# Kernel optimization log

Hardware: AMD Instinct MI355X
Metric: run time of the kernel (lower is better)

The kernel has to match this reference:

```python
import jax, jax.numpy as jnp
import numpy as np

TEMP = 0.07  # softmax temperature T


def _l2norm(x, axis=1, eps=1e-12):
    return x / jnp.clip(jnp.linalg.norm(x, axis=axis, keepdims=True), eps, None)


def setup_inputs() -> dict:
    key = jax.random.key(0)
    k1, k2, k3, k4 = jax.random.split(key, 4)
    B, K, D = 256, 8192, 128
    q = jax.random.normal(k1, (B, D), dtype=jnp.float32)
    ba_queue = _l2norm(jax.random.normal(k2, (K, D), dtype=jnp.float32))
    nonba_queue = _l2norm(jax.random.normal(k3, (K, D), dtype=jnp.float32))
    targets = jax.random.randint(k4, (B,), 0, 2, dtype=jnp.int64)
    return {"q": q, "ba_queue": ba_queue, "nonba_queue": nonba_queue, "targets": targets}


def reference(q, ba_queue, nonba_queue, targets):
    K = ba_queue.shape[0]
    # encoder output is L2-normalized; queues are detached buffers
    qn = _l2norm(q, axis=1)
    all_feature = jnp.concatenate([qn, ba_queue, nonba_queue], axis=0)  # [N, D]
    all_label = jnp.concatenate([
        targets.astype(jnp.int32),
        jnp.ones((K,), dtype=jnp.int32),
        jnp.zeros((K,), dtype=jnp.int32),
    ])  # [N]
    N = all_feature.shape[0]

    # [N, N] similarity logits
    sim = jnp.matmul(all_feature, all_feature.T) / TEMP
    logits = sim - jax.lax.stop_gradient(jnp.max(sim, axis=1, keepdims=True))

    # positive mask (same label), excluding self
    mask = (all_label[:, None] == all_label[None, :]).astype(jnp.float32)
    logits_mask = 1.0 - jnp.eye(N, dtype=jnp.float32)
    mask = mask * logits_mask

    exp_logits = jnp.exp(logits) * logits_mask
    log_prob = logits - jnp.log(jnp.sum(exp_logits, axis=1, keepdims=True))
    mean_log_prob_pos = jnp.sum(mask * log_prob, axis=1) / jnp.sum(mask, axis=1)
    return -jnp.mean(mean_log_prob_pos)
```

## Files before the change

kernel.cpp:

```cpp
#include <hip/hip_runtime.h>
#include <hip/hip_bf16.h>
#include <stdint.h>

#define TEMPERATURE 0.07f
#define SC 20.6099312f

constexpr int NQ = 256;
constexpr int KQ = 8192;
constexpr int D  = 128;
constexpr int N  = NQ + 2 * KQ;
constexpr int CS = 26;
constexpr int CS2 = CS * 2;
constexpr int BN = 128;
constexpr int RBM = N / 128;
constexpr int RBF = N / 256;

typedef float f32x16 __attribute__((ext_vector_type(16)));
typedef int   i32x4  __attribute__((ext_vector_type(4)));
typedef int   i32x8  __attribute__((ext_vector_type(8)));

constexpr size_t OFF_F32  = 0;
constexpr size_t OFF_8    = OFF_F32  + (size_t)NQ * D * 4;
constexpr size_t OFF_8S   = OFF_8    + (size_t)N * D;
constexpr size_t OFF_PART = OFF_8S   + (size_t)N * D;
constexpr size_t OFF_LP   = OFF_PART + (size_t)CS2 * N * 4;
constexpr size_t OFF_BSUM = OFF_LP   + (size_t)260 * 2 * 128 * 4;

#define MFMA8(a, b, c) __builtin_amdgcn_mfma_scale_f32_32x32x64_f8f6f4( \
    (a), (b), (c), 0, 0, 0, 0x7f7f7f7f, 0, 0x7f7f7f7f)

__global__ __launch_bounds__(256) void k_prep(const float* __restrict__ q,
                                              const float* __restrict__ ba,
                                              const float* __restrict__ nb,
                                              const long long* __restrict__ tgt,
                                              float* __restrict__ ff,
                                              unsigned char* __restrict__ fb8,
                                              unsigned char* __restrict__ fb8s,
                                              float* __restrict__ lp) {
    __shared__ float red[4][2][128];
    int wid = threadIdx.x >> 6, lane = threadIdx.x & 63;
    int rbase = blockIdx.x * 64 + wid * 16;
    float s0x = 0.f, s0y = 0.f, s1x = 0.f, s1y = 0.f;
    for (int i = 0; i < 16; ++i) {
        int r = rbase + i;
        const float* src = (r < NQ) ? (q + (size_t)r * D)
                         : (r < NQ + KQ) ? (ba + (size_t)(r - NQ) * D)
                         : (nb + (size_t)(r - NQ - KQ) * D);
        float2 v = *(const float2*)(src + lane * 2);
        float a = v.x, b = v.y;
        int lab;
        if (r < NQ) {
            float ss = a * a + b * b;
            #pragma unroll
            for (int m = 1; m < 64; m <<= 1) ss += __shfl_xor(ss, m);
            float scale = 1.0f / fmaxf(sqrtf(ss), 1e-12f);
            a *= scale; b *= scale;
            lab = (int)tgt[r];
            *(float2*)(ff + (size_t)r * D + lane * 2) = make_float2(a, b);
        } else {
            lab = (r < NQ + KQ) ? 1 : 0;
        }
        int w8  = __builtin_amdgcn_cvt_pk_fp8_f32(a, b, 0, false);
        int w8s = __builtin_amdgcn_cvt_pk_fp8_f32(a * SC, b * SC, 0, false);
        *(unsigned short*)(fb8  + (size_t)r * D + lane * 2) = (unsigned short)w8;
        *(unsigned short*)(fb8s + (size_t)r * D + lane * 2) = (unsigned short)w8s;
        if (lab) { s1x += a; s1y += b; } else { s0x += a; s0y += b; }
    }
    red[wid][0][lane * 2]     = s0x;
    red[wid][0][lane * 2 + 1] = s0y;
    red[wid][1][lane * 2]     = s1x;
    red[wid][1][lane * 2 + 1] = s1y;
    __syncthreads();
    int lab2 = threadIdx.x >> 7, d = threadIdx.x & 127;
    float s = red[0][lab2][d] + red[1][lab2][d] + red[2][lab2][d] + red[3][lab2][d];
    lp[((size_t)blockIdx.x * 2 + lab2) * 128 + d] = s;
}

__global__ __launch_bounds__(256, 4) void k_main(const unsigned char* __restrict__ fb8,
                                                 const unsigned char* __restrict__ fb8s,
                                                 float* __restrict__ part) {
    __shared__ __align__(16) unsigned char lds[2][BN * 128];
    const int bid = blockIdx.x;
    const int rb = bid / CS, cs = bid % CS;
    const int tid = threadIdx.x;
    const int lane = tid & 63;
    const int wid  = tid >> 6;
    const int wr = wid >> 1, wc = wid & 1;
    const int l31 = lane & 31, lhi = lane >> 5;
    const int rw = rb * 128 + wr * 64;

    int soff[4];
    #pragma unroll
    for (int i = 0; i < 4; ++i) {
        int flat = i * 256 + tid;
        int line = flat >> 4, p = flat & 15;
        int pl = p ^ (line & 15);
        soff[i] = (2 * line + (pl >> 3)) * 128 + (pl & 7) * 16;
    }

#define STAGE(T, B) { \
    const unsigned char* base_ = fb8 + ((size_t)(cs + (T) * CS)) * (BN * 128); \
    _Pragma("unroll") \
    for (int i_ = 0; i_ < 4; ++i_) \
        __builtin_amdgcn_global_load_lds( \
            (const __attribute__((address_space(1))) unsigned int*)(base_ + soff[i_]), \
            (__attribute__((address_space(3))) unsigned int*)(&lds[B][(i_ * 256 + tid) * 16]), \
            16, 0, 0); }

#define SYNC() { asm volatile("s_waitcnt vmcnt(0)" ::: "memory"); __builtin_amdgcn_s_barrier(); }

    i32x8 rf[2][2];
    #pragma unroll
    for (int rs = 0; rs < 2; ++rs)
        #pragma unroll
        for (int s = 0; s < 2; ++s)
            rf[rs][s] = *(const i32x8*)(fb8s + (size_t)(rw + rs * 32 + l31) * D + s * 64 + lhi * 32);

    f32x16 z16;
    #pragma unroll
    for (int e = 0; e < 16; ++e) z16[e] = 0.f;

    float2 ps2[2] = {{0.f, 0.f}, {0.f, 0.f}};

    STAGE(0, 0) SYNC()

    #pragma unroll 1
    for (int t = 0; t < 5; ++t) {
        if (t + 1 < 5) STAGE(t + 1, (t & 1) ^ 1)
        const unsigned char* buf = &lds[t & 1][0];

        f32x16 acc[2][2];
        __builtin_amdgcn_s_setprio(1);
        #pragma unroll
        for (int s = 0; s < 2; ++s) {
            #pragma unroll
            for (int cc = 0; cc < 2; ++cc) {
                int crow = wc * 64 + cc * 32 + l31;
                int line = crow >> 1;
                int pb = ((crow & 1) << 3) + s * 4 + lhi * 2;
                const unsigned char* lb = buf + line * 256;
                i32x4 lo = *(const i32x4*)(lb + ((pb    ) ^ (line & 15)) * 16);
                i32x4 hi = *(const i32x4*)(lb + ((pb + 1) ^ (line & 15)) * 16);
                i32x8 a = {lo[0], lo[1], lo[2], lo[3], hi[0], hi[1], hi[2], hi[3]};
                acc[cc][0] = MFMA8(a, rf[0][s], (s == 0) ? z16 : acc[cc][0]);
                acc[cc][1] = MFMA8(a, rf[1][s], (s == 0) ? z16 : acc[cc][1]);
            }
        }
        __builtin_amdgcn_s_setprio(0);

        #pragma unroll
        for (int cc = 0; cc < 2; ++cc)
            #pragma unroll
            for (int rs = 0; rs < 2; ++rs) {
                float2 p = {0.f, 0.f};
                #pragma unroll
                for (int g = 0; g < 8; ++g) {
                    p.x += __builtin_amdgcn_exp2f(acc[cc][rs][2 * g]);
                    p.y += __builtin_amdgcn_exp2f(acc[cc][rs][2 * g + 1]);
                }
                ps2[rs].x += p.x; ps2[rs].y += p.y;
            }

        SYNC()
    }

    float rsum[2] = {ps2[0].x + ps2[0].y, ps2[1].x + ps2[1].y};
    rsum[0] += __shfl_xor(rsum[0], 32);
    rsum[1] += __shfl_xor(rsum[1], 32);
    if (lane < 32) {
        float* dst = part + (size_t)(cs * 2 + wc) * N + rw + lane;
        dst[0]  = rsum[0];
        dst[32] = rsum[1];
    }
#undef STAGE
#undef SYNC
}

__global__ __launch_bounds__(256) void k_rowfin(const float* __restrict__ part,
                                                const float* __restrict__ ff,
                                                const float* __restrict__ ba,
                                                const float* __restrict__ nb,
                                                const float* __restrict__ lp,
                                                const long long* __restrict__ tgt,
                                                float* __restrict__ bsum) {
    __shared__ float sS[256];
    __shared__ float red[256];
    __shared__ int scnt[2];
    {
        int lab = threadIdx.x >> 7, d = threadIdx.x & 127;
        float s[4] = {0.f, 0.f, 0.f, 0.f};
        for (int b = 0; b < 260; b += 4) {
            #pragma unroll
            for (int j = 0; j < 4; ++j)
                s[j] += lp[((size_t)(b + j) * 2 + lab) * 128 + d];
        }
        sS[threadIdx.x] = (s[0] + s[1]) + (s[2] + s[3]);
        if (threadIdx.x < 64) {
            int c = 0;
            #pragma unroll
            for (int i = 0; i < 4; ++i) c += (int)tgt[threadIdx.x + 64 * i];
            #pragma unroll
            for (int m = 1; m < 64; m <<= 1) c += __shfl_xor(c, m);
            if (threadIdx.x == 0) { scnt[0] = (NQ - c) + KQ; scnt[1] = c + KQ; }
        }
    }
    __syncthreads();
    int r = blockIdx.x * 256 + threadIdx.x;
    float se = 0.f;
    #pragma unroll 4
    for (int c = 0; c < CS2; ++c) se += part[(size_t)c * N + r];
    int lab = (r < NQ) ? (int)tgt[r] : ((r < NQ + KQ) ? 1 : 0);
    const float* fsrc = (r < NQ) ? (ff + (size_t)r * D)
                      : (r < NQ + KQ) ? (ba + (size_t)(r - NQ) * D)
                      : (nb + (size_t)(r - NQ - KQ) * D);
    const float4* frow = (const float4*)fsrc;
    const float4* srow = (const float4*)(sS + lab * 128);
    float dS = 0.f, dd = 0.f;
    #pragma unroll
    for (int i = 0; i < 32; ++i) {
        float4 f = frow[i];
        float4 s = srow[i];
        dS += f.x * s.x + f.y * s.y + f.z * s.z + f.w * s.w;
        int wa  = __builtin_amdgcn_cvt_pk_fp8_f32(f.x, f.y, 0, false);
        int wb  = __builtin_amdgcn_cvt_pk_fp8_f32(f.z, f.w, 0, false);
        int wsa = __builtin_amdgcn_cvt_pk_fp8_f32(f.x * SC, f.y * SC, 0, false);
        int wsb = __builtin_amdgcn_cvt_pk_fp8_f32(f.z * SC, f.w * SC, 0, false);
        dd += __builtin_amdgcn_cvt_f32_fp8(wa, 0) * __builtin_amdgcn_cvt_f32_fp8(wsa, 0)
            + __builtin_amdgcn_cvt_f32_fp8(wa, 1) * __builtin_amdgcn_cvt_f32_fp8(wsa, 1)
            + __builtin_amdgcn_cvt_f32_fp8(wb, 0) * __builtin_amdgcn_cvt_f32_fp8(wsb, 0)
            + __builtin_amdgcn_cvt_f32_fp8(wb, 1) * __builtin_amdgcn_cvt_f32_fp8(wsb, 1);
    }
    se -= __builtin_amdgcn_exp2f(dd);
    float lse = logf(se);
    float P = (float)(scnt[lab] - 1);
    float mlpp = (dS - 1.0f) / (TEMPERATURE * P) - lse;
    red[threadIdx.x] = mlpp;
    __syncthreads();
    for (int s2 = 128; s2 > 0; s2 >>= 1) {
        if (threadIdx.x < s2) red[threadIdx.x] += red[threadIdx.x + s2];
        __syncthreads();
    }
    if (threadIdx.x == 0) bsum[blockIdx.x] = red[0];
}

__global__ __launch_bounds__(64) void k_final(const float* __restrict__ bsum,
                                              float* __restrict__ out) {
    float s = bsum[threadIdx.x];
    if (threadIdx.x == 0) s += bsum[64];
    #pragma unroll
    for (int m = 1; m < 64; m <<= 1) s += __shfl_xor(s, m);
    if (threadIdx.x == 0) out[0] = -s / (float)N;
}

extern "C" void kernel_launch(void* const* d_in, const int* in_sizes, int n_in,
                              void* d_out, int out_size, void* d_ws, size_t ws_size,
                              hipStream_t stream) {
    const float* q       = (const float*)d_in[0];
    const float* ba      = (const float*)d_in[1];
    const float* nb      = (const float*)d_in[2];
    const long long* tgt = (const long long*)d_in[3];
    char* ws = (char*)d_ws;
    float*         ff   = (float*)(ws + OFF_F32);
    unsigned char* fb8  = (unsigned char*)(ws + OFF_8);
    unsigned char* fb8s = (unsigned char*)(ws + OFF_8S);
    float*         part = (float*)(ws + OFF_PART);
    float*         lp   = (float*)(ws + OFF_LP);
    float*         bsum = (float*)(ws + OFF_BSUM);

    k_prep  <<<260,      256, 0, stream>>>(q, ba, nb, tgt, ff, fb8, fb8s, lp);
    k_main  <<<RBM * CS, 256, 0, stream>>>(fb8, fb8s, part);
    k_rowfin<<<RBF,      256, 0, stream>>>(part, ff, ba, nb, lp, tgt, bsum);
    k_final <<<1,         64, 0, stream>>>(bsum, (float*)d_out);
}
```

Measured before the change: 82.23 us.

## Make each wave an independent job with private LDS buffers, removing block barriers

The main similarity kernel now gives each wavefront its own 64-row by column-split job, with a private double-buffered 4KB LDS stage in place of a 128x128 tile shared by the block. Block-wide barriers are gone and each wave waits only on its own loads through vmcnt counts. The number of column splits doubles to 52 and the grid grows to 3380 blocks. This drops per-tile barrier stalls and lets waves run out of sync, but it gives up sharing a staged tile across the four waves, so global and L2 traffic per MFMA rises.

```diff
diff --git a/kernel.cpp b/kernel.cpp
--- a/kernel.cpp
+++ b/kernel.cpp
@@ -9,10 +9,8 @@
 constexpr int KQ = 8192;
 constexpr int D  = 128;
 constexpr int N  = NQ + 2 * KQ;
-constexpr int CS = 26;
-constexpr int CS2 = CS * 2;
-constexpr int BN = 128;
-constexpr int RBM = N / 128;
+constexpr int CSW = 52;
+constexpr int NTW = 520 / CSW;
 constexpr int RBF = N / 256;
 
 typedef float f32x16 __attribute__((ext_vector_type(16)));
@@ -23,7 +21,7 @@
 constexpr size_t OFF_8    = OFF_F32  + (size_t)NQ * D * 4;
 constexpr size_t OFF_8S   = OFF_8    + (size_t)N * D;
 constexpr size_t OFF_PART = OFF_8S   + (size_t)N * D;
-constexpr size_t OFF_LP   = OFF_PART + (size_t)CS2 * N * 4;
+constexpr size_t OFF_LP   = OFF_PART + (size_t)CSW * N * 4;
 constexpr size_t OFF_BSUM = OFF_LP   + (size_t)260 * 2 * 128 * 4;
 
 #define MFMA8(a, b, c) __builtin_amdgcn_mfma_scale_f32_32x32x64_f8f6f4( \
@@ -79,35 +77,40 @@
 __global__ __launch_bounds__(256, 4) void k_main(const unsigned char* __restrict__ fb8,
                                                  const unsigned char* __restrict__ fb8s,
                                                  float* __restrict__ part) {
-    __shared__ __align__(16) unsigned char lds[2][BN * 128];
-    const int bid = blockIdx.x;
-    const int rb = bid / CS, cs = bid % CS;
+    __shared__ __align__(16) unsigned char lds[4][2][4096];
     const int tid = threadIdx.x;
     const int lane = tid & 63;
     const int wid  = tid >> 6;
-    const int wr = wid >> 1, wc = wid & 1;
+    const int job  = blockIdx.x * 4 + wid;
+    const int rg = job / CSW, cs = job % CSW;
     const int l31 = lane & 31, lhi = lane >> 5;
-    const int rw = rb * 128 + wr * 64;
+    const int rw = rg * 64;
+
+    unsigned char* myl = &lds[wid][0][0];
 
     int soff[4];
     #pragma unroll
     for (int i = 0; i < 4; ++i) {
-        int flat = i * 256 + tid;
-        int line = flat >> 4, p = flat & 15;
-        int pl = p ^ (line & 15);
-        soff[i] = (2 * line + (pl >> 3)) * 128 + (pl & 7) * 16;
+        int f = i * 64 + lane;
+        int row = f >> 3, pslot = f & 7;
+        soff[i] = row * 128 + ((pslot ^ (row & 7)) << 4);
+    }
+    int lofs[2][2];
+    #pragma unroll
+    for (int s = 0; s < 2; ++s) {
+        int p = s * 4 + lhi * 2;
+        lofs[s][0] = (l31 * 8 + ((p)     ^ (l31 & 7))) * 16;
+        lofs[s][1] = (l31 * 8 + ((p + 1) ^ (l31 & 7))) * 16;
     }
 
 #define STAGE(T, B) { \
-    const unsigned char* base_ = fb8 + ((size_t)(cs + (T) * CS)) * (BN * 128); \
+    const unsigned char* base_ = fb8 + ((size_t)(cs + (T) * CSW)) * 4096; \
     _Pragma("unroll") \
     for (int i_ = 0; i_ < 4; ++i_) \
         __builtin_amdgcn_global_load_lds( \
             (const __attribute__((address_space(1))) unsigned int*)(base_ + soff[i_]), \
-            (__attribute__((address_space(3))) unsigned int*)(&lds[B][(i_ * 256 + tid) * 16]), \
+            (__attribute__((address_space(3))) unsigned int*)(myl + (B) * 4096 + (i_ * 64 + lane) * 16), \
             16, 0, 0); }
-
-#define SYNC() { asm volatile("s_waitcnt vmcnt(0)" ::: "memory"); __builtin_amdgcn_s_barrier(); }
 
     i32x8 rf[2][2];
     #pragma unroll
@@ -122,58 +125,51 @@
 
     float2 ps2[2] = {{0.f, 0.f}, {0.f, 0.f}};
 
-    STAGE(0, 0) SYNC()
+    STAGE(0, 0)
 
     #pragma unroll 1
-    for (int t = 0; t < 5; ++t) {
-        if (t + 1 < 5) STAGE(t + 1, (t & 1) ^ 1)
-        const unsigned char* buf = &lds[t & 1][0];
-
-        f32x16 acc[2][2];
+    for (int t = 0; t < NTW; ++t) {
+        if (t + 1 < NTW) {
+            STAGE(t + 1, (t & 1) ^ 1)
+            asm volatile("s_waitcnt vmcnt(4)" ::: "memory");
+        } else {
+            asm volatile("s_waitcnt vmcnt(0)" ::: "memory");
+        }
+        const unsigned char* buf = myl + (t & 1) * 4096;
+
+        f32x16 acc[2];
         __builtin_amdgcn_s_setprio(1);
         #pragma unroll
         for (int s = 0; s < 2; ++s) {
-            #pragma unroll
-            for (int cc = 0; cc < 2; ++cc) {
-                int crow = wc * 64 + cc * 32 + l31;
-                int line = crow >> 1;
-                int pb = ((crow & 1) << 3) + s * 4 + lhi * 2;
-                const unsigned char* lb = buf + line * 256;
-                i32x4 lo = *(const i32x4*)(lb + ((pb    ) ^ (line & 15)) * 16);
-                i32x4 hi = *(const i32x4*)(lb + ((pb + 1) ^ (line & 15)) * 16);
-                i32x8 a = {lo[0], lo[1], lo[2], lo[3], hi[0], hi[1], hi[2], hi[3]};
-                acc[cc][0] = MFMA8(a, rf[0][s], (s == 0) ? z16 : acc[cc][0]);
-                acc[cc][1] = MFMA8(a, rf[1][s], (s == 0) ? z16 : acc[cc][1]);
+            i32x4 lo = *(const i32x4*)(buf + lofs[s][0]);
+            i32x4 hi = *(const i32x4*)(buf + lofs[s][1]);
+            i32x8 a = {lo[0], lo[1], lo[2], lo[3], hi[0], hi[1], hi[2], hi[3]};
+            acc[0] = MFMA8(a, rf[0][s], (s == 0) ? z16 : acc[0]);
+            acc[1] = MFMA8(a, rf[1][s], (s == 0) ? z16 : acc[1]);
+        }
+        __builtin_amdgcn_s_setprio(0);
+
+        #pragma unroll
+        for (int rs = 0; rs < 2; ++rs) {
+            float2 p = {0.f, 0.f};
+            #pragma unroll
+            for (int g = 0; g < 8; ++g) {
+                p.x += __builtin_amdgcn_exp2f(acc[rs][2 * g]);
+                p.y += __builtin_amdgcn_exp2f(acc[rs][2 * g + 1]);
             }
-        }
-        __builtin_amdgcn_s_setprio(0);
-
-        #pragma unroll
-        for (int cc = 0; cc < 2; ++cc)
-            #pragma unroll
-            for (int rs = 0; rs < 2; ++rs) {
-                float2 p = {0.f, 0.f};
-                #pragma unroll
-                for (int g = 0; g < 8; ++g) {
-                    p.x += __builtin_amdgcn_exp2f(acc[cc][rs][2 * g]);
-                    p.y += __builtin_amdgcn_exp2f(acc[cc][rs][2 * g + 1]);
-                }
-                ps2[rs].x += p.x; ps2[rs].y += p.y;
-            }
-
-        SYNC()
-    }
-
-    float rsum[2] = {ps2[0].x + ps2[0].y, ps2[1].x + ps2[1].y};
-    rsum[0] += __shfl_xor(rsum[0], 32);
-    rsum[1] += __shfl_xor(rsum[1], 32);
+            ps2[rs].x += p.x; ps2[rs].y += p.y;
+        }
+    }
+
+    float rsum0 = ps2[0].x + ps2[0].y;
+    float rsum1 = ps2[1].x + ps2[1].y;
+    rsum0 += __shfl_xor(rsum0, 32);
+    rsum1 += __shfl_xor(rsum1, 32);
     if (lane < 32) {
-        float* dst = part + (size_t)(cs * 2 + wc) * N + rw + lane;
-        dst[0]  = rsum[0];
-        dst[32] = rsum[1];
+        part[(size_t)cs * N + rw + lane]      = rsum0;
+        part[(size_t)cs * N + rw + 32 + lane] = rsum1;
     }
 #undef STAGE
-#undef SYNC
 }
 
 __global__ __launch_bounds__(256) void k_rowfin(const float* __restrict__ part,
@@ -208,7 +204,7 @@
     int r = blockIdx.x * 256 + threadIdx.x;
     float se = 0.f;
     #pragma unroll 4
-    for (int c = 0; c < CS2; ++c) se += part[(size_t)c * N + r];
+    for (int c = 0; c < CSW; ++c) se += part[(size_t)c * N + r];
     int lab = (r < NQ) ? (int)tgt[r] : ((r < NQ + KQ) ? 1 : 0);
     const float* fsrc = (r < NQ) ? (ff + (size_t)r * D)
                       : (r < NQ + KQ) ? (ba + (size_t)(r - NQ) * D)
@@ -267,8 +263,8 @@
     float*         lp   = (float*)(ws + OFF_LP);
     float*         bsum = (float*)(ws + OFF_BSUM);
 
-    k_prep  <<<260,      256, 0, stream>>>(q, ba, nb, tgt, ff, fb8, fb8s, lp);
-    k_main  <<<RBM * CS, 256, 0, stream>>>(fb8, fb8s, part);
-    k_rowfin<<<RBF,      256, 0, stream>>>(part, ff, ba, nb, lp, tgt, bsum);
-    k_final <<<1,         64, 0, stream>>>(bsum, (float*)d_out);
-}
+    k_prep  <<<260,  256, 0, stream>>>(q, ba, nb, tgt, ff, fb8, fb8s, lp);
+    k_main  <<<3380, 256, 0, stream>>>(fb8, fb8s, part);
+    k_rowfin<<<RBF,  256, 0, stream>>>(part, ff, ba, nb, lp, tgt, bsum);
+    k_final <<<1,     64, 0, stream>>>(bsum, (float*)d_out);
+}
```

After: 87.57 us. 6.5% more time.

## Replace partial-sum buffers and final kernel with fixed-point atomics

Applied to the files above, without the earlier changes.

k_prep now runs twice as many blocks, each handling half as many rows. Its per-label feature sums are accumulated into a 64-bit fixed-point global buffer with atomics, replacing the per-block partials that k_rowfin used to reduce. k_rowfin now adds its block total atomically and the last-arriving block writes the final loss, so the separate k_final launch is gone. A memset launch is added to clear the accumulators, and the fixed-point scaling could lose precision or overflow.

```diff
diff --git a/kernel.cpp b/kernel.cpp
--- a/kernel.cpp
+++ b/kernel.cpp
@@ -14,6 +14,7 @@
 constexpr int BN = 128;
 constexpr int RBM = N / 128;
 constexpr int RBF = N / 256;
+constexpr int PB = 520;
 
 typedef float f32x16 __attribute__((ext_vector_type(16)));
 typedef int   i32x4  __attribute__((ext_vector_type(4)));
@@ -23,8 +24,8 @@
 constexpr size_t OFF_8    = OFF_F32  + (size_t)NQ * D * 4;
 constexpr size_t OFF_8S   = OFF_8    + (size_t)N * D;
 constexpr size_t OFF_PART = OFF_8S   + (size_t)N * D;
-constexpr size_t OFF_LP   = OFF_PART + (size_t)CS2 * N * 4;
-constexpr size_t OFF_BSUM = OFF_LP   + (size_t)260 * 2 * 128 * 4;
+constexpr size_t OFF_ATOM = OFF_PART + (size_t)CS2 * N * 4;
+constexpr size_t ATOM_BYTES = 256 * 8 + 16;
 
 #define MFMA8(a, b, c) __builtin_amdgcn_mfma_scale_f32_32x32x64_f8f6f4( \
     (a), (b), (c), 0, 0, 0, 0x7f7f7f7f, 0, 0x7f7f7f7f)
@@ -36,12 +37,13 @@
                                               float* __restrict__ ff,
                                               unsigned char* __restrict__ fb8,
                                               unsigned char* __restrict__ fb8s,
-                                              float* __restrict__ lp) {
+                                              unsigned long long* __restrict__ iS) {
     __shared__ float red[4][2][128];
     int wid = threadIdx.x >> 6, lane = threadIdx.x & 63;
-    int rbase = blockIdx.x * 64 + wid * 16;
+    int rbase = blockIdx.x * 32 + wid * 8;
     float s0x = 0.f, s0y = 0.f, s1x = 0.f, s1y = 0.f;
-    for (int i = 0; i < 16; ++i) {
+    #pragma unroll
+    for (int i = 0; i < 8; ++i) {
         int r = rbase + i;
         const float* src = (r < NQ) ? (q + (size_t)r * D)
                          : (r < NQ + KQ) ? (ba + (size_t)(r - NQ) * D)
@@ -73,7 +75,8 @@
     __syncthreads();
     int lab2 = threadIdx.x >> 7, d = threadIdx.x & 127;
     float s = red[0][lab2][d] + red[1][lab2][d] + red[2][lab2][d] + red[3][lab2][d];
-    lp[((size_t)blockIdx.x * 2 + lab2) * 128 + d] = s;
+    long long fx = __double2ll_rn((double)s * 4294967296.0);
+    atomicAdd(&iS[lab2 * 128 + d], (unsigned long long)fx);
 }
 
 __global__ __launch_bounds__(256, 4) void k_main(const unsigned char* __restrict__ fb8,
@@ -180,29 +183,20 @@
                                                 const float* __restrict__ ff,
                                                 const float* __restrict__ ba,
                                                 const float* __restrict__ nb,
-                                                const float* __restrict__ lp,
+                                                unsigned long long* __restrict__ atom,
                                                 const long long* __restrict__ tgt,
-                                                float* __restrict__ bsum) {
+                                                float* __restrict__ out) {
     __shared__ float sS[256];
     __shared__ float red[256];
     __shared__ int scnt[2];
-    {
-        int lab = threadIdx.x >> 7, d = threadIdx.x & 127;
-        float s[4] = {0.f, 0.f, 0.f, 0.f};
-        for (int b = 0; b < 260; b += 4) {
-            #pragma unroll
-            for (int j = 0; j < 4; ++j)
-                s[j] += lp[((size_t)(b + j) * 2 + lab) * 128 + d];
-        }
-        sS[threadIdx.x] = (s[0] + s[1]) + (s[2] + s[3]);
-        if (threadIdx.x < 64) {
-            int c = 0;
-            #pragma unroll
-            for (int i = 0; i < 4; ++i) c += (int)tgt[threadIdx.x + 64 * i];
-            #pragma unroll
-            for (int m = 1; m < 64; m <<= 1) c += __shfl_xor(c, m);
-            if (threadIdx.x == 0) { scnt[0] = (NQ - c) + KQ; scnt[1] = c + KQ; }
-        }
+    sS[threadIdx.x] = (float)((double)(long long)atom[threadIdx.x] * (1.0 / 4294967296.0));
+    if (threadIdx.x < 64) {
+        int c = 0;
+        #pragma unroll
+        for (int i = 0; i < 4; ++i) c += (int)tgt[threadIdx.x + 64 * i];
+        #pragma unroll
+        for (int m = 1; m < 64; m <<= 1) c += __shfl_xor(c, m);
+        if (threadIdx.x == 0) { scnt[0] = (NQ - c) + KQ; scnt[1] = c + KQ; }
     }
     __syncthreads();
     int r = blockIdx.x * 256 + threadIdx.x;
@@ -240,16 +234,19 @@
         if (threadIdx.x < s2) red[threadIdx.x] += red[threadIdx.x + s2];
         __syncthreads();
     }
-    if (threadIdx.x == 0) bsum[blockIdx.x] = red[0];
-}
-
-__global__ __launch_bounds__(64) void k_final(const float* __restrict__ bsum,
-                                              float* __restrict__ out) {
-    float s = bsum[threadIdx.x];
-    if (threadIdx.x == 0) s += bsum[64];
-    #pragma unroll
-    for (int m = 1; m < 64; m <<= 1) s += __shfl_xor(s, m);
-    if (threadIdx.x == 0) out[0] = -s / (float)N;
+    if (threadIdx.x == 0) {
+        unsigned long long* lacc = atom + 256;
+        unsigned long long* done = atom + 257;
+        long long fx = __double2ll_rn((double)red[0] * 16777216.0);
+        atomicAdd(lacc, (unsigned long long)fx);
+        __threadfence();
+        unsigned long long old = atomicAdd(done, 1ull);
+        if (old == (unsigned long long)(RBF - 1)) {
+            __threadfence();
+            long long tot = (long long)atomicAdd(lacc, 0ull);
+            out[0] = (float)(-((double)tot * (1.0 / 16777216.0)) / (double)N);
+        }
+    }
 }
 
 extern "C" void kernel_launch(void* const* d_in, const int* in_sizes, int n_in,
@@ -260,15 +257,14 @@
     const float* nb      = (const float*)d_in[2];
     const long long* tgt = (const long long*)d_in[3];
     char* ws = (char*)d_ws;
-    float*         ff   = (float*)(ws + OFF_F32);
-    unsigned char* fb8  = (unsigned char*)(ws + OFF_8);
-    unsigned char* fb8s = (unsigned char*)(ws + OFF_8S);
-    float*         part = (float*)(ws + OFF_PART);
-    float*         lp   = (float*)(ws + OFF_LP);
-    float*         bsum = (float*)(ws + OFF_BSUM);
-
-    k_prep  <<<260,      256, 0, stream>>>(q, ba, nb, tgt, ff, fb8, fb8s, lp);
+    float*              ff   = (float*)(ws + OFF_F32);
+    unsigned char*      fb8  = (unsigned char*)(ws + OFF_8);
+    unsigned char*      fb8s = (unsigned char*)(ws + OFF_8S);
+    float*              part = (float*)(ws + OFF_PART);
+    unsigned long long* atom = (unsigned long long*)(ws + OFF_ATOM);
+
+    hipMemsetAsync(atom, 0, ATOM_BYTES, stream);
+    k_prep  <<<PB,       256, 0, stream>>>(q, ba, nb, tgt, ff, fb8, fb8s, atom);
     k_main  <<<RBM * CS, 256, 0, stream>>>(fb8, fb8s, part);
-    k_rowfin<<<RBF,      256, 0, stream>>>(part, ff, ba, nb, lp, tgt, bsum);
-    k_final <<<1,         64, 0, stream>>>(bsum, (float*)d_out);
-}
+    k_rowfin<<<RBF,      256, 0, stream>>>(part, ff, ba, nb, atom, tgt, (float*)d_out);
+}
```

Result: slower. 84.09 us (+2.3%).
